# Kernel optimization log

Hardware: AMD Instinct MI355X
Metric: run time of the kernel (lower is better)

## Reference

```python
import jax, jax.numpy as jnp
import numpy as np

B, S, D, H = 4, 2048, 1024, 16
DK = D // H

def setup_inputs() -> dict:
    key = jax.random.key(0)
    ks = jax.random.split(key, 13)
    std = 1.0 / np.sqrt(D)
    inp = {
        'query': jax.random.normal(ks[0], (B, S, D), jnp.float32),
        'key':   jax.random.normal(ks[1], (B, S, D), jnp.float32),
        'value': jax.random.normal(ks[2], (B, S, D), jnp.float32),
        'mask':  jax.random.randint(ks[3], (B, 1, S), 0, 2, jnp.int32),
        'Wq': jax.random.normal(ks[4], (D, D), jnp.float32) * std,
        'bq': jnp.zeros((D,), jnp.float32),
        'Wk': jax.random.normal(ks[5], (D, D), jnp.float32) * std,
        'bk': jnp.zeros((D,), jnp.float32),
        'Wv': jax.random.normal(ks[6], (D, D), jnp.float32) * std,
        'bv': jnp.zeros((D,), jnp.float32),
        'Wo': jax.random.normal(ks[7], (D, D), jnp.float32) * std,
        'bo': jnp.zeros((D,), jnp.float32),
    }
    return inp

def reference(query, key, value, mask, Wq, bq, Wk, bk, Wv, bv, Wo, bo):
    # QKV projections (torch Linear: x @ W.T + b), reshape to [B,H,S,DK]
    def proj(x, W, b):
        y = x @ W.T + b
        return y.reshape(B, S, H, DK).transpose(0, 2, 1, 3)
    q = proj(query, Wq, bq)
    k = proj(key, Wk, bk)
    v = proj(value, Wv, bv)
    scores = jnp.einsum('bhqd,bhkd->bhqk', q, k) / jnp.sqrt(jnp.float32(DK))
    # mask [B,1,S] -> unsqueeze head dim -> [B,1,1,S], broadcast over h,q
    m = mask[:, None, :, :]  # [B,1,1,S]
    scores = jnp.where(m == 0, jnp.float32(-1e9), scores)
    p = jax.nn.softmax(scores, axis=-1)  # dropout omitted (eval mode)
    x = jnp.einsum('bhqk,bhkd->bhqd', p, v)
    x = x.transpose(0, 2, 1, 3).reshape(B, S, D)
    return x @ Wo.T + bo
```

## Files before the change

kernel.cpp:

```cpp
#include <hip/hip_runtime.h>

typedef unsigned short u16;
typedef unsigned int u32;
typedef __bf16 bf16x8 __attribute__((ext_vector_type(8)));
typedef float f32x4 __attribute__((ext_vector_type(4)));
typedef u16 u16x8 __attribute__((ext_vector_type(8)));
typedef u16 u16x4 __attribute__((ext_vector_type(4)));

typedef __attribute__((address_space(1))) const unsigned char gc_u8;
typedef __attribute__((address_space(3))) unsigned char lds_u8;

__device__ inline void gload16(const void* g, void* l) {
    __builtin_amdgcn_global_load_lds((gc_u8*)g, (lds_u8*)l, 16, 0, 0);
}
__device__ inline u16 f2bf(float f) {
    union { __bf16 h; u16 u; } c; c.h = (__bf16)f; return c.u;
}
__device__ inline float bf2f(u16 u) {
    union { u16 u[2]; float f; } c; c.u[0] = 0; c.u[1] = u; return c.f;
}
__device__ inline void hard_barrier() {
    __builtin_amdgcn_sched_barrier(0);
    __builtin_amdgcn_s_barrier();
    __builtin_amdgcn_sched_barrier(0);
}
#define WAIT_LGKM0() asm volatile("s_waitcnt lgkmcnt(0)" ::: "memory")
#define WAIT_VMCNT(n) asm volatile("s_waitcnt vmcnt(" #n ")" ::: "memory")

__global__ __launch_bounds__(256) void cvt4(const float* __restrict__ s0,
                                            const float* __restrict__ s1,
                                            const float* __restrict__ s2,
                                            const float* __restrict__ s3,
                                            u16* __restrict__ d0, u16* __restrict__ d1,
                                            u16* __restrict__ d2, u16* __restrict__ d3,
                                            int n) {
    const int y = blockIdx.y;
    const float* src = (y == 0) ? s0 : (y == 1) ? s1 : (y == 2) ? s2 : s3;
    u16* dst = (y == 0) ? d0 : (y == 1) ? d1 : (y == 2) ? d2 : d3;
    int i = (blockIdx.x * 256 + threadIdx.x) * 4;
    if (i < n) {
        float4 f = *reinterpret_cast<const float4*>(src + i);
        u16x4 u = { f2bf(f.x), f2bf(f.y), f2bf(f.z), f2bf(f.w) };
        *reinterpret_cast<u16x4*>(dst + i) = u;
    }
}

__global__ __launch_bounds__(256) void zero_buf(u16* __restrict__ p) {
    const size_t i = ((size_t)blockIdx.x * 256 + threadIdx.x) * 8;
    u16x8 z = {0, 0, 0, 0, 0, 0, 0, 0};
    *(u16x8*)&p[i] = z;
}

__global__ __launch_bounds__(256) void build_dtok(const int* __restrict__ mask,
                                                  int* __restrict__ dtok,
                                                  int* __restrict__ NbA) {
    __shared__ u32 W[64];
    __shared__ u32 Wpre[64];
    const int b = blockIdx.x, t = threadIdx.x;
    const int* mrow = mask + b * 2048;
    if (t < 64) {
        u32 wv = 0;
#pragma unroll 8
        for (int j = 0; j < 32; j++) wv |= (mrow[t * 32 + j] ? 1u : 0u) << j;
        W[t] = wv;
    }
    __syncthreads();
    if (t == 0) {
        u32 s = 0;
        for (int i = 0; i < 64; i++) { Wpre[i] = s; s += __popc(W[i]); }
        NbA[b] = (int)s;
    }
    __syncthreads();
#pragma unroll
    for (int i = 0; i < 8; i++) {
        const int s = t * 8 + i;
        const u32 word = W[s >> 5];
        const int d = (int)Wpre[s >> 5] + __popc(word & ((1u << (s & 31)) - 1u));
        dtok[b * 2048 + s] = ((word >> (s & 31)) & 1u) ? d : -1;
    }
}

__global__ __launch_bounds__(256) void gemm_qkv(const float* __restrict__ Aq,
                                                const float* __restrict__ Ak,
                                                const float* __restrict__ Av,
                                                const u16* __restrict__ Bq,
                                                const u16* __restrict__ Bk,
                                                const u16* __restrict__ Bv,
                                                const float* __restrict__ bq,
                                                const float* __restrict__ bk,
                                                const float* __restrict__ bv,
                                                const int* __restrict__ dtok,
                                                u16* __restrict__ Cq,
                                                u16* __restrict__ Ck,
                                                u16* __restrict__ Cvp,
                                                int M, int N, int K) {
    __shared__ __align__(16) float Asf[2][128][32];
    __shared__ __align__(16) u16 Bs[2][128][32];
    const int z = blockIdx.z;
    const float* A = (z == 0) ? Aq : (z == 1) ? Ak : Av;
    const u16* B = (z == 0) ? Bq : (z == 1) ? Bk : Bv;
    const float* bias = (z == 0) ? bq : (z == 1) ? bk : bv;

    const int t = threadIdx.x, lane = t & 63, w = t >> 6;
    const int wr = w >> 1, wc = w & 1;
    const int l15 = lane & 15, l16 = lane >> 4;
    const int nwg = gridDim.x, ntiles = N >> 7;
    const int wg = blockIdx.x, chunk = nwg >> 3;
    const int swz = (wg & 7) * chunk + (wg >> 3);
    const int bm = (swz / ntiles) * 128, bn = (swz % ntiles) * 128;
    const int srow = w * 16 + (lane >> 2);
    const int sgr = (lane & 3) * 8;
    const int arsub = lane >> 3;
    const int agr = ((lane & 7) ^ (lane >> 3)) * 4;
    const u16* Bb = B + (size_t)bn * K;

    f32x4 acc[4][4];
#pragma unroll
    for (int i = 0; i < 4; i++)
#pragma unroll
        for (int j = 0; j < 4; j++) acc[i][j] = (f32x4){0.f, 0.f, 0.f, 0.f};

    auto stage = [&](int c, int k0) {
#pragma unroll
        for (int ch = 0; ch < 4; ch++)
            gload16(A + (size_t)(bm + ch * 32 + w * 8 + arsub) * K + k0 + agr,
                    &Asf[c][ch * 32 + w * 8][0]);
        gload16(Bb + (size_t)srow * K + k0 + sgr,        &Bs[c][w * 16][0]);
        gload16(Bb + (size_t)(64 + srow) * K + k0 + sgr, &Bs[c][64 + w * 16][0]);
    };

    stage(0, 0);
    __syncthreads();

    const int NS = K >> 5;
    for (int i = 0; i < NS; ++i) {
        const int c = i & 1;
        WAIT_LGKM0();
        hard_barrier();
        if (i + 1 < NS) {
            stage(c ^ 1, (i + 1) * 32);
            WAIT_VMCNT(6);
        } else {
            WAIT_VMCNT(0);
        }
        hard_barrier();

        const int key = l15 & 7;
        bf16x8 afr[4], bfr[4];
#pragma unroll
        for (int mi = 0; mi < 4; mi++) {
            const int rr = wr * 64 + mi * 16 + l15;
            f32x4 lo = *(const f32x4*)&Asf[c][rr][((2 * l16) ^ key) * 4];
            f32x4 hi = *(const f32x4*)&Asf[c][rr][((2 * l16 + 1) ^ key) * 4];
            bf16x8 v;
            v[0] = (__bf16)lo[0]; v[1] = (__bf16)lo[1];
            v[2] = (__bf16)lo[2]; v[3] = (__bf16)lo[3];
            v[4] = (__bf16)hi[0]; v[5] = (__bf16)hi[1];
            v[6] = (__bf16)hi[2]; v[7] = (__bf16)hi[3];
            afr[mi] = v;
        }
#pragma unroll
        for (int ni = 0; ni < 4; ni++)
            bfr[ni] = *(const bf16x8*)&Bs[c][wc * 64 + ni * 16 + l15][l16 * 8];
#pragma unroll
        for (int mi = 0; mi < 4; mi++)
#pragma unroll
            for (int ni = 0; ni < 4; ni++)
                acc[mi][ni] = __builtin_amdgcn_mfma_f32_16x16x32_bf16(
                    afr[mi], bfr[ni], acc[mi][ni], 0, 0, 0);
    }

    int dts[4][4];
    if (z != 0) {
#pragma unroll
        for (int mi = 0; mi < 4; mi++) {
            const int r0 = bm + wr * 64 + mi * 16 + l16 * 4;
#pragma unroll
            for (int r = 0; r < 4; r++) dts[mi][r] = dtok[r0 + r];
        }
    }

#pragma unroll
    for (int ni = 0; ni < 4; ni++) {
        const int col = bn + wc * 64 + ni * 16 + l15;
        const float bv2 = bias[col];
#pragma unroll
        for (int mi = 0; mi < 4; mi++) {
            const int r0 = bm + wr * 64 + mi * 16 + l16 * 4;
            const int bb = r0 >> 11;
            if (z == 0) {
#pragma unroll
                for (int r = 0; r < 4; r++)
                    Cq[(size_t)(r0 + r) * N + col] = f2bf(acc[mi][ni][r] + bv2);
            } else if (z == 1) {
#pragma unroll
                for (int r = 0; r < 4; r++) {
                    const int d = dts[mi][r];
                    if (d >= 0)
                        Ck[((size_t)(bb * 2048 + d)) * 1024 + col] =
                            f2bf(acc[mi][ni][r] + bv2);
                }
            } else {
                const int hh = col >> 6, dk = col & 63;
                u16* dst = Cvp + (((size_t)(bb * 16 + hh) * 64 + dk) << 11);
#pragma unroll
                for (int r = 0; r < 4; r++) {
                    const int d = dts[mi][r];
                    if (d >= 0) dst[d] = f2bf(acc[mi][ni][r] + bv2);
                }
            }
        }
    }
}

__global__ __launch_bounds__(256) void gemm_out(const u16* __restrict__ A,
                                                const u16* __restrict__ B,
                                                const float* __restrict__ bias,
                                                float* __restrict__ Cv,
                                                int M, int N, int K) {
    __shared__ __align__(16) u16 As[2][128][32];
    __shared__ __align__(16) u16 Bs[2][128][32];
    const int t = threadIdx.x, lane = t & 63, w = t >> 6;
    const int wr = w >> 1, wc = w & 1;
    const int l15 = lane & 15, l16 = lane >> 4;
    const int nwg = gridDim.x, ntiles = N >> 7;
    const int wg = blockIdx.x, chunk = nwg >> 3;
    const int swz = (wg & 7) * chunk + (wg >> 3);
    const int bm = (swz / ntiles) * 128, bn = (swz % ntiles) * 128;
    const int srow = w * 16 + (lane >> 2);
    const int sgr = (lane & 3) * 8;
    const u16* Ab = A + (size_t)bm * K;
    const u16* Bb = B + (size_t)bn * K;

    f32x4 acc[4][4];
#pragma unroll
    for (int i = 0; i < 4; i++)
#pragma unroll
        for (int j = 0; j < 4; j++) acc[i][j] = (f32x4){0.f, 0.f, 0.f, 0.f};

    auto stage = [&](int c, int k0) {
        gload16(Ab + (size_t)srow * K + k0 + sgr,        &As[c][w * 16][0]);
        gload16(Ab + (size_t)(64 + srow) * K + k0 + sgr, &As[c][64 + w * 16][0]);
        gload16(Bb + (size_t)srow * K + k0 + sgr,        &Bs[c][w * 16][0]);
        gload16(Bb + (size_t)(64 + srow) * K + k0 + sgr, &Bs[c][64 + w * 16][0]);
    };

    stage(0, 0);
    __syncthreads();

    const int NS = K >> 5;
    for (int i = 0; i < NS; ++i) {
        const int c = i & 1;
        WAIT_LGKM0();
        hard_barrier();
        if (i + 1 < NS) {
            stage(c ^ 1, (i + 1) * 32);
            WAIT_VMCNT(4);
        } else {
            WAIT_VMCNT(0);
        }
        hard_barrier();

        bf16x8 afr[4], bfr[4];
#pragma unroll
        for (int mi = 0; mi < 4; mi++)
            afr[mi] = *(const bf16x8*)&As[c][wr * 64 + mi * 16 + l15][l16 * 8];
#pragma unroll
        for (int ni = 0; ni < 4; ni++)
            bfr[ni] = *(const bf16x8*)&Bs[c][wc * 64 + ni * 16 + l15][l16 * 8];
#pragma unroll
        for (int mi = 0; mi < 4; mi++)
#pragma unroll
            for (int ni = 0; ni < 4; ni++)
                acc[mi][ni] = __builtin_amdgcn_mfma_f32_16x16x32_bf16(
                    afr[mi], bfr[ni], acc[mi][ni], 0, 0, 0);
    }

#pragma unroll
    for (int ni = 0; ni < 4; ni++) {
        const int col = bn + wc * 64 + ni * 16 + l15;
        const float bv = bias[col];
#pragma unroll
        for (int mi = 0; mi < 4; mi++) {
            const int r0 = bm + wr * 64 + mi * 16 + l16 * 4;
#pragma unroll
            for (int r = 0; r < 4; r++)
                Cv[(size_t)(r0 + r) * N + col] = acc[mi][ni][r] + bv;
        }
    }
}

__global__ __launch_bounds__(256, 2) void attn_fwd(const u16* __restrict__ Q,
                                                   const u16* __restrict__ Kg,
                                                   const u16* __restrict__ Vt,
                                                   const int* __restrict__ NbA,
                                                   u16* __restrict__ O) {
    constexpr int S = 2048, D = 1024;
    __shared__ __align__(16) u16 Kl[2][2][2][64][32];
    __shared__ __align__(16) u16 Vl[2][2][2][64][32];
    __shared__ __align__(16) u16 Pl[4][16][68];
    __shared__ __align__(16) u16 Ml[2048];
    const int t = threadIdx.x, lane = t & 63, w = t >> 6;
    const int l15 = lane & 15, l16 = lane >> 4;
    const int wg = blockIdx.x;
    const int swz = (wg & 7) * 64 + (wg >> 3);
    const int q0 = (swz & 7) * 256, hd = (swz >> 3) & 15, b = swz >> 7;
    const int qb = q0 + w * 64;
    const int srow = w * 16 + (lane >> 2);
    const int sgr = ((lane & 3) ^ ((lane >> 3) & 3)) * 8;
    const int gsw8 = (l16 ^ ((l15 >> 1) & 3)) * 8;

    const int Nb = NbA[b];
    const int nt = (Nb + 127) >> 7;

    const u16* Khead = Kg + (size_t)b * S * D;
    const u16* Vthead = Vt + (size_t)(b * 16 + hd) * 64 * 2048;

    auto stage = [&](int c, int kt) {
#pragma unroll
        for (int kg = 0; kg < 2; kg++) {
            const int k0 = kt + kg * 64;
            gload16(Khead + (size_t)(k0 + srow) * D + hd * 64 + sgr,      &Kl[c][kg][0][w * 16][0]);
            gload16(Khead + (size_t)(k0 + srow) * D + hd * 64 + 32 + sgr, &Kl[c][kg][1][w * 16][0]);
            gload16(Vthead + (size_t)srow * 2048 + k0 + sgr,              &Vl[c][kg][0][w * 16][0]);
            gload16(Vthead + (size_t)srow * 2048 + k0 + 32 + sgr,         &Vl[c][kg][1][w * 16][0]);
        }
    };

    stage(0, 0);
    {
        u16x8 mv;
#pragma unroll
        for (int j = 0; j < 8; j++) mv[j] = (t * 8 + j < Nb) ? (u16)0x3F80 : (u16)0;
        *(u16x8*)&Ml[t * 8] = mv;
    }

    constexpr float QSCALE = 0.125f * 1.44269504f;
    bf16x8 aq[4][2];
#pragma unroll
    for (int qt = 0; qt < 4; qt++)
#pragma unroll
        for (int ks = 0; ks < 2; ks++) {
            const size_t qi = ((size_t)b * S + qb + qt * 16 + l15) * D +
                              hd * 64 + ks * 32 + l16 * 8;
            u16x8 raw = *(const u16x8*)&Q[qi];
            bf16x8 qv;
#pragma unroll
            for (int i = 0; i < 8; i++) qv[i] = (__bf16)(bf2f(raw[i]) * QSCALE);
            aq[qt][ks] = qv;
        }

    f32x4 acc[4][4];
    f32x4 accl[4];
#pragma unroll
    for (int qt = 0; qt < 4; qt++) {
        accl[qt] = (f32x4){0.f, 0.f, 0.f, 0.f};
#pragma unroll
        for (int dt = 0; dt < 4; dt++) acc[qt][dt] = (f32x4){0.f, 0.f, 0.f, 0.f};
    }

    __syncthreads();

    for (int tile = 0; tile < nt; ++tile) {
        const int c = tile & 1;
        const int cur = tile * 128;
        WAIT_LGKM0();
        hard_barrier();
        if (tile + 1 < nt) {
            stage(c ^ 1, cur + 128);
            WAIT_VMCNT(8);
        } else {
            WAIT_VMCNT(0);
        }
        hard_barrier();

#pragma unroll
        for (int kg = 0; kg < 2; kg++) {
            bf16x8 kf0[4], kf1[4], vf0[4], vf1[4];
#pragma unroll
            for (int k4 = 0; k4 < 4; k4++) {
                kf0[k4] = *(const bf16x8*)&Kl[c][kg][0][k4 * 16 + l15][gsw8];
                kf1[k4] = *(const bf16x8*)&Kl[c][kg][1][k4 * 16 + l15][gsw8];
            }
#pragma unroll
            for (int dt = 0; dt < 4; dt++) {
                vf0[dt] = *(const bf16x8*)&Vl[c][kg][0][dt * 16 + l15][gsw8];
                vf1[dt] = *(const bf16x8*)&Vl[c][kg][1][dt * 16 + l15][gsw8];
            }
            const int kbase = cur + kg * 64;
            bf16x8 mv0 = *(const bf16x8*)&Ml[kbase + l16 * 8];
            bf16x8 mv1 = *(const bf16x8*)&Ml[kbase + 32 + l16 * 8];

#pragma unroll
            for (int qt = 0; qt < 4; qt++) {
#pragma unroll
                for (int k4 = 0; k4 < 4; k4++) {
                    f32x4 z = (f32x4){0.f, 0.f, 0.f, 0.f};
                    z = __builtin_amdgcn_mfma_f32_16x16x32_bf16(kf0[k4], aq[qt][0], z, 0, 0, 0);
                    z = __builtin_amdgcn_mfma_f32_16x16x32_bf16(kf1[k4], aq[qt][1], z, 0, 0, 0);
                    u16x4 pk;
#pragma unroll
                    for (int r = 0; r < 4; r++)
                        pk[r] = f2bf(__builtin_amdgcn_exp2f(z[r]));
                    *(u16x4*)&Pl[w][l15][k4 * 16 + l16 * 4] = pk;
                }
                bf16x8 pa0 = *(const bf16x8*)&Pl[w][l15][l16 * 8];
                bf16x8 pa1 = *(const bf16x8*)&Pl[w][l15][32 + l16 * 8];
                accl[qt] = __builtin_amdgcn_mfma_f32_16x16x32_bf16(pa0, mv0, accl[qt], 0, 0, 0);
                accl[qt] = __builtin_amdgcn_mfma_f32_16x16x32_bf16(pa1, mv1, accl[qt], 0, 0, 0);
#pragma unroll
                for (int dt = 0; dt < 4; dt++) {
                    acc[qt][dt] = __builtin_amdgcn_mfma_f32_16x16x32_bf16(
                        pa0, vf0[dt], acc[qt][dt], 0, 0, 0);
                    acc[qt][dt] = __builtin_amdgcn_mfma_f32_16x16x32_bf16(
                        pa1, vf1[dt], acc[qt][dt], 0, 0, 0);
                }
            }
        }
    }

#pragma unroll
    for (int qt = 0; qt < 4; qt++) {
        f32x4 inv;
#pragma unroll
        for (int r = 0; r < 4; r++) inv[r] = 1.f / accl[qt][r];
#pragma unroll
        for (int dt = 0; dt < 4; dt++)
#pragma unroll
            for (int r = 0; r < 4; r++) {
                const int tok = qb + qt * 16 + l16 * 4 + r;
                O[((size_t)b * S + tok) * D + hd * 64 + dt * 16 + l15] =
                    f2bf(acc[qt][dt][r] * inv[r]);
            }
    }
}

extern "C" void kernel_launch(void* const* d_in, const int* in_sizes, int n_in,
                              void* d_out, int out_size, void* d_ws, size_t ws_size,
                              hipStream_t stream) {
    const float* query = (const float*)d_in[0];
    const float* key   = (const float*)d_in[1];
    const float* value = (const float*)d_in[2];
    const int*   mask  = (const int*)d_in[3];
    const float* Wq = (const float*)d_in[4];
    const float* bq = (const float*)d_in[5];
    const float* Wk = (const float*)d_in[6];
    const float* bk = (const float*)d_in[7];
    const float* Wv = (const float*)d_in[8];
    const float* bv = (const float*)d_in[9];
    const float* Wo = (const float*)d_in[10];
    const float* bo = (const float*)d_in[11];
    float* out = (float*)d_out;

    constexpr int S = 2048, D = 1024;
    constexpr size_t MSZ = (size_t)4 * S * D;
    constexpr size_t WSZ = (size_t)D * D;
    const size_t need = 4 * WSZ * 2 + 4 * MSZ * 2 + 8192 * 4 + 64;
    if (ws_size < need) return;

    char* p = (char*)d_ws;
    u16* Wqb = (u16*)p; p += WSZ * 2;
    u16* Wkb = (u16*)p; p += WSZ * 2;
    u16* Wvb = (u16*)p; p += WSZ * 2;
    u16* Wob = (u16*)p; p += WSZ * 2;
    u16* Xb  = (u16*)p; p += MSZ * 2;
    u16* Qb  = (u16*)p; p += MSZ * 2;
    u16* KbUnused = (u16*)p; p += MSZ * 2;
    u16* VtUnused = (u16*)p; p += MSZ * 2;
    int* dtok = (int*)p; p += 8192 * 4;
    int* NbA = (int*)p; p += 64;
    (void)KbUnused; (void)VtUnused;
    u16* Kc  = (u16*)d_out;
    u16* Vtc = (u16*)d_out + MSZ;

    cvt4<<<dim3(WSZ / 1024, 4), 256, 0, stream>>>(Wq, Wk, Wv, Wo,
                                                  Wqb, Wkb, Wvb, Wob, (int)WSZ);
    build_dtok<<<4, 256, 0, stream>>>(mask, dtok, NbA);
    zero_buf<<<8192, 256, 0, stream>>>((u16*)d_out);
    gemm_qkv<<<dim3(512, 1, 3), 256, 0, stream>>>(query, key, value,
                                                  Wqb, Wkb, Wvb, bq, bk, bv, dtok,
                                                  Qb, Kc, Vtc, 8192, 1024, 1024);
    attn_fwd<<<512, 256, 0, stream>>>(Qb, Kc, Vtc, NbA, Xb);
    gemm_out<<<512, 256, 0, stream>>>(Xb, Wob, bo, out, 8192, 1024, 1024);
}
```

Measured before the change: 183.9 us.

## Drop zero-fill kernel by writing pad zeros in QKV epilogue; swizzle LDS B tiles

Removes the separate zero_buf kernel, which cleared the whole 32MB compacted K/V scratch. Instead build_dtok encodes, for masked tokens, a slot in the padding region up to the next multiple of 128. The gemm_qkv epilogue writes zeros there, so only the padding that attention actually reads gets cleared. It also applies an XOR swizzle to the bf16 LDS tiles in gemm_qkv's B operand and both gemm_out operands to reduce bank conflicts on the fragment reads. In exchange, the correctness of the padded rows now depends on the compaction encoding, and the epilogue gains extra branches.

Result: faster. 179.0 us, median of 2 (-2.7%).

```diff
diff --git a/kernel.cpp b/kernel.cpp
--- a/kernel.cpp
+++ b/kernel.cpp
@@ -45,17 +45,11 @@
     }
 }
 
-__global__ __launch_bounds__(256) void zero_buf(u16* __restrict__ p) {
-    const size_t i = ((size_t)blockIdx.x * 256 + threadIdx.x) * 8;
-    u16x8 z = {0, 0, 0, 0, 0, 0, 0, 0};
-    *(u16x8*)&p[i] = z;
-}
-
 __global__ __launch_bounds__(256) void build_dtok(const int* __restrict__ mask,
                                                   int* __restrict__ dtok,
                                                   int* __restrict__ NbA) {
     __shared__ u32 W[64];
-    __shared__ u32 Wpre[64];
+    __shared__ u32 Wpre[65];
     const int b = blockIdx.x, t = threadIdx.x;
     const int* mrow = mask + b * 2048;
     if (t < 64) {
@@ -68,15 +62,25 @@
     if (t == 0) {
         u32 s = 0;
         for (int i = 0; i < 64; i++) { Wpre[i] = s; s += __popc(W[i]); }
+        Wpre[64] = s;
         NbA[b] = (int)s;
     }
     __syncthreads();
+    const int Nb = (int)Wpre[64];
+    const int pad = (Nb + 127) & ~127;
 #pragma unroll
     for (int i = 0; i < 8; i++) {
         const int s = t * 8 + i;
         const u32 word = W[s >> 5];
-        const int d = (int)Wpre[s >> 5] + __popc(word & ((1u << (s & 31)) - 1u));
-        dtok[b * 2048 + s] = ((word >> (s & 31)) & 1u) ? d : -1;
+        const int pre = (int)Wpre[s >> 5] + __popc(word & ((1u << (s & 31)) - 1u));
+        int v;
+        if ((word >> (s & 31)) & 1u) {
+            v = pre;
+        } else {
+            const int slot = Nb + (s - pre);
+            v = (slot < pad) ? -(slot + 2) : -1;
+        }
+        dtok[b * 2048 + s] = v;
     }
 }
 
@@ -109,7 +113,8 @@
     const int swz = (wg & 7) * chunk + (wg >> 3);
     const int bm = (swz / ntiles) * 128, bn = (swz % ntiles) * 128;
     const int srow = w * 16 + (lane >> 2);
-    const int sgr = (lane & 3) * 8;
+    const int sgrB = ((lane & 3) ^ ((lane >> 3) & 3)) * 8;
+    const int gswB = (l16 ^ ((l15 >> 1) & 3)) * 8;
     const int arsub = lane >> 3;
     const int agr = ((lane & 7) ^ (lane >> 3)) * 4;
     const u16* Bb = B + (size_t)bn * K;
@@ -125,8 +130,8 @@
         for (int ch = 0; ch < 4; ch++)
             gload16(A + (size_t)(bm + ch * 32 + w * 8 + arsub) * K + k0 + agr,
                     &Asf[c][ch * 32 + w * 8][0]);
-        gload16(Bb + (size_t)srow * K + k0 + sgr,        &Bs[c][w * 16][0]);
-        gload16(Bb + (size_t)(64 + srow) * K + k0 + sgr, &Bs[c][64 + w * 16][0]);
+        gload16(Bb + (size_t)srow * K + k0 + sgrB,        &Bs[c][w * 16][0]);
+        gload16(Bb + (size_t)(64 + srow) * K + k0 + sgrB, &Bs[c][64 + w * 16][0]);
     };
 
     stage(0, 0);
@@ -161,7 +166,7 @@
         }
 #pragma unroll
         for (int ni = 0; ni < 4; ni++)
-            bfr[ni] = *(const bf16x8*)&Bs[c][wc * 64 + ni * 16 + l15][l16 * 8];
+            bfr[ni] = *(const bf16x8*)&Bs[c][wc * 64 + ni * 16 + l15][gswB];
 #pragma unroll
         for (int mi = 0; mi < 4; mi++)
 #pragma unroll
@@ -199,6 +204,8 @@
                     if (d >= 0)
                         Ck[((size_t)(bb * 2048 + d)) * 1024 + col] =
                             f2bf(acc[mi][ni][r] + bv2);
+                    else if (d != -1)
+                        Ck[((size_t)(bb * 2048 + (-d - 2))) * 1024 + col] = 0;
                 }
             } else {
                 const int hh = col >> 6, dk = col & 63;
@@ -207,6 +214,7 @@
                 for (int r = 0; r < 4; r++) {
                     const int d = dts[mi][r];
                     if (d >= 0) dst[d] = f2bf(acc[mi][ni][r] + bv2);
+                    else if (d != -1) dst[-d - 2] = 0;
                 }
             }
         }
@@ -228,7 +236,8 @@
     const int swz = (wg & 7) * chunk + (wg >> 3);
     const int bm = (swz / ntiles) * 128, bn = (swz % ntiles) * 128;
     const int srow = w * 16 + (lane >> 2);
-    const int sgr = (lane & 3) * 8;
+    const int sgrB = ((lane & 3) ^ ((lane >> 3) & 3)) * 8;
+    const int gswB = (l16 ^ ((l15 >> 1) & 3)) * 8;
     const u16* Ab = A + (size_t)bm * K;
     const u16* Bb = B + (size_t)bn * K;
 
@@ -239,10 +248,10 @@
         for (int j = 0; j < 4; j++) acc[i][j] = (f32x4){0.f, 0.f, 0.f, 0.f};
 
     auto stage = [&](int c, int k0) {
-        gload16(Ab + (size_t)srow * K + k0 + sgr,        &As[c][w * 16][0]);
-        gload16(Ab + (size_t)(64 + srow) * K + k0 + sgr, &As[c][64 + w * 16][0]);
-        gload16(Bb + (size_t)srow * K + k0 + sgr,        &Bs[c][w * 16][0]);
-        gload16(Bb + (size_t)(64 + srow) * K + k0 + sgr, &Bs[c][64 + w * 16][0]);
+        gload16(Ab + (size_t)srow * K + k0 + sgrB,        &As[c][w * 16][0]);
+        gload16(Ab + (size_t)(64 + srow) * K + k0 + sgrB, &As[c][64 + w * 16][0]);
+        gload16(Bb + (size_t)srow * K + k0 + sgrB,        &Bs[c][w * 16][0]);
+        gload16(Bb + (size_t)(64 + srow) * K + k0 + sgrB, &Bs[c][64 + w * 16][0]);
     };
 
     stage(0, 0);
@@ -264,10 +273,10 @@
         bf16x8 afr[4], bfr[4];
 #pragma unroll
         for (int mi = 0; mi < 4; mi++)
-            afr[mi] = *(const bf16x8*)&As[c][wr * 64 + mi * 16 + l15][l16 * 8];
+            afr[mi] = *(const bf16x8*)&As[c][wr * 64 + mi * 16 + l15][gswB];
 #pragma unroll
         for (int ni = 0; ni < 4; ni++)
-            bfr[ni] = *(const bf16x8*)&Bs[c][wc * 64 + ni * 16 + l15][l16 * 8];
+            bfr[ni] = *(const bf16x8*)&Bs[c][wc * 64 + ni * 16 + l15][gswB];
 #pragma unroll
         for (int mi = 0; mi < 4; mi++)
 #pragma unroll
@@ -455,7 +464,7 @@
     constexpr int S = 2048, D = 1024;
     constexpr size_t MSZ = (size_t)4 * S * D;
     constexpr size_t WSZ = (size_t)D * D;
-    const size_t need = 4 * WSZ * 2 + 4 * MSZ * 2 + 8192 * 4 + 64;
+    const size_t need = 4 * WSZ * 2 + 2 * MSZ * 2 + 8192 * 4 + 64;
     if (ws_size < need) return;
 
     char* p = (char*)d_ws;
@@ -465,18 +474,14 @@
     u16* Wob = (u16*)p; p += WSZ * 2;
     u16* Xb  = (u16*)p; p += MSZ * 2;
     u16* Qb  = (u16*)p; p += MSZ * 2;
-    u16* KbUnused = (u16*)p; p += MSZ * 2;
-    u16* VtUnused = (u16*)p; p += MSZ * 2;
     int* dtok = (int*)p; p += 8192 * 4;
     int* NbA = (int*)p; p += 64;
-    (void)KbUnused; (void)VtUnused;
     u16* Kc  = (u16*)d_out;
     u16* Vtc = (u16*)d_out + MSZ;
 
     cvt4<<<dim3(WSZ / 1024, 4), 256, 0, stream>>>(Wq, Wk, Wv, Wo,
                                                   Wqb, Wkb, Wvb, Wob, (int)WSZ);
     build_dtok<<<4, 256, 0, stream>>>(mask, dtok, NbA);
-    zero_buf<<<8192, 256, 0, stream>>>((u16*)d_out);
     gemm_qkv<<<dim3(512, 1, 3), 256, 0, stream>>>(query, key, value,
                                                   Wqb, Wkb, Wvb, bq, bk, bv, dtok,
                                                   Qb, Kc, Vtc, 8192, 1024, 1024);
```
